# Optimization experiments

Measured on AMD Instinct MI355X. Metric: run time of the kernel, lower is better.

The kernel has to match this reference:

```python
import jax, jax.numpy as jnp
import numpy as np

LAM = 0.5          # lambda_ in DyGCN
GROUPS = 4
EPS_GN = 1e-5
EPS_LN = 1e-5


def _group_norm(y, w, b):
    # y: [B, Ch, N, T]; GroupNorm over (channels-in-group, N, T)
    B, Ch, N, T = y.shape
    yr = y.reshape(B, GROUPS, Ch // GROUPS, N, T)
    mu = yr.mean(axis=(2, 3, 4), keepdims=True)
    var = yr.var(axis=(2, 3, 4), keepdims=True)
    yn = ((yr - mu) * jax.lax.rsqrt(var + EPS_GN)).reshape(B, Ch, N, T)
    return yn * w[None, :, None, None] + b[None, :, None, None]


def _gtu(X, w, b, pw, pb, qw, qb):
    # grouped conv2d, kernel (1,k), stride 1, VALID; out channels = 2*H
    xc = jax.lax.conv_general_dilated(
        X, w, window_strides=(1, 1), padding='VALID',
        feature_group_count=GROUPS,
        dimension_numbers=('NCHW', 'OIHW', 'NCHW'))
    xc = xc + b[None, :, None, None]
    H = X.shape[1]
    xp = _group_norm(xc[:, :H], pw, pb)   # matches torch chunk(2, dim=1)
    xq = _group_norm(xc[:, H:], qw, qb)
    mish = xp * jnp.tanh(jax.nn.softplus(xp))   # Mish
    gate = jnp.clip(xq, 0.0, 1.0)               # Hardtanh(0,1)
    return mish * gate


def reference(x, static_adj, U1, U2, U3, be, Ve, W0, b0, masks, Ws, bs, Wd, bd,
              conv3_w, conv5_w, conv7_w, conv9_w, conv_b,
              gn_pw, gn_pb, gn_qw, gn_qb, fc_w, fc_b, res_w, res_b, ln_w, ln_b):
    B, N, C, T = x.shape
    # ---- Temporal attention ----
    lhs = jnp.einsum('btc,cn->btn', jnp.einsum('bnct,n->btc', x, U1), U2)  # [B,T,N]
    rhs = jnp.einsum('c,bnct->bnt', U3, x)                                 # [B,N,T]
    product = jnp.einsum('btn,bns->bts', lhs, rhs)                          # [B,T,T]
    E = jnp.einsum('ij,bjk->bik', Ve, jax.nn.sigmoid(product + be))
    At = jax.nn.softmax(E, axis=1)
    x_TAt = jnp.einsum('bmt,bts->bms', x.reshape(B, N * C, T), At).reshape(B, N, C, T)
    # ---- DyGCN, vectorized across T ----
    xt = jnp.moveaxis(x_TAt, -1, 1)                                        # [B,T,N,C]
    x0 = jnp.einsum('btnc,hc->btnh', xt, W0) + b0                          # shared linear
    enh = static_adj[None] * jax.nn.sigmoid(masks)                         # [T,N,N]
    s = jnp.einsum('tnm,btmc->btnc', enh, xt)
    static_out = jnp.einsum('btnc,thc->btnh', s, Ws) + bs[None, :, None, :]
    # dynamic branch (DynamicGCNLayer): data-dependent adjacency
    scores = jnp.einsum('btnc,btmc->btnm', xt, xt) / jnp.sqrt(jnp.float32(C))
    adj = jax.nn.softmax(scores, axis=-1)                                  # [B,T,N,N]
    d = jnp.einsum('btnm,btmc->btnc', adj, xt)
    dyn_out = jnp.einsum('btnc,thc->btnh', d, Wd) + bd[None, :, None, :]
    fused = (LAM - 0.025) * static_out + (1.0 - LAM - 0.025) * dyn_out + 0.05 * x0
    X = jnp.transpose(fused, (0, 3, 2, 1))                                 # [B,H,N,T]
    # ---- multi-scale gated temporal convs ----
    outs = [
        _gtu(X, conv3_w, conv_b[0], gn_pw[0], gn_pb[0], gn_qw[0], gn_qb[0]),
        _gtu(X, conv5_w, conv_b[1], gn_pw[1], gn_pb[1], gn_qw[1], gn_qb[1]),
        _gtu(X, conv7_w, conv_b[2], gn_pw[2], gn_pb[2], gn_qw[2], gn_qb[2]),
        _gtu(X, conv9_w, conv_b[3], gn_pw[3], gn_pb[3], gn_qw[3], gn_qb[3]),
    ]
    tc = jnp.concatenate(outs, axis=-1)                                    # [B,H,N,4T-20]
    tc = jnp.einsum('bhnk,ok->bhno', tc, fc_w) + fc_b                      # fcmy (dropout=eval no-op)
    tco = jax.nn.relu(tc)                                                  # [B,H,N,T]
    # ---- residual + LayerNorm ----
    residual = jnp.einsum('bnct,hc->bhnt', x, res_w) + res_b[None, :, None, None]
    y = jax.nn.relu(residual + tco)                                        # [B,H,N,T]
    yp = jnp.transpose(y, (0, 3, 2, 1))                                    # [B,T,N,H]
    mu = yp.mean(axis=-1, keepdims=True)
    var = yp.var(axis=-1, keepdims=True)
    yn = (yp - mu) * jax.lax.rsqrt(var + EPS_LN) * ln_w + ln_b
    return jnp.transpose(yn, (0, 2, 3, 1))                                 # [B,N,H,T]


def setup_inputs():
    key = jax.random.key(0)
    ks = jax.random.split(key, 32)
    B, N, C, T, H = 16, 512, 64, 12, 64
    w = 0.05
    A = jax.random.uniform(ks[0], (N, N), jnp.float32)
    A = A / A.sum(axis=-1, keepdims=True)  # row-normalized static adjacency
    return {
        'x': jax.random.normal(ks[1], (B, N, C, T), jnp.float32),
        'static_adj': A,
        'U1': jax.random.normal(ks[2], (N,), jnp.float32) * w,
        'U2': jax.random.normal(ks[3], (C, N), jnp.float32) * w,
        'U3': jax.random.normal(ks[4], (C,), jnp.float32) * w,
        'be': jax.random.normal(ks[5], (1, T, T), jnp.float32) * w,
        'Ve': jax.random.normal(ks[6], (T, T), jnp.float32) * w,
        'W0': jax.random.normal(ks[7], (H, C), jnp.float32) * w,
        'b0': jnp.zeros((H,), jnp.float32),
        'masks': jax.random.uniform(ks[8], (T, N, N), jnp.float32, 0.8, 1.2),
        'Ws': jax.random.normal(ks[9], (T, H, C), jnp.float32) * w,
        'bs': jnp.zeros((T, H), jnp.float32),
        'Wd': jax.random.normal(ks[10], (T, H, C), jnp.float32) * w,
        'bd': jnp.zeros((T, H), jnp.float32),
        'conv3_w': jax.random.normal(ks[11], (2 * H, H // 4, 1, 3), jnp.float32) * w,
        'conv5_w': jax.random.normal(ks[12], (2 * H, H // 4, 1, 5), jnp.float32) * w,
        'conv7_w': jax.random.normal(ks[13], (2 * H, H // 4, 1, 7), jnp.float32) * w,
        'conv9_w': jax.random.normal(ks[14], (2 * H, H // 4, 1, 9), jnp.float32) * w,
        'conv_b': jnp.zeros((4, 2 * H), jnp.float32),
        'gn_pw': jnp.ones((4, H), jnp.float32),
        'gn_pb': jnp.zeros((4, H), jnp.float32),
        'gn_qw': jnp.ones((4, H), jnp.float32),
        'gn_qb': jnp.zeros((4, H), jnp.float32),
        'fc_w': jax.random.normal(ks[15], (T, 4 * T - 20), jnp.float32) * w,
        'fc_b': jnp.zeros((T,), jnp.float32),
        'res_w': jax.random.normal(ks[16], (H, C), jnp.float32) * w,
        'res_b': jnp.zeros((H,), jnp.float32),
        'ln_w': jnp.ones((H,), jnp.float32),
        'ln_b': jnp.zeros((H,), jnp.float32),
    }
```

## Files before the change

### kernel.cpp

```cpp
#include <hip/hip_runtime.h>

constexpr int Bb = 16, Nn = 512, Cc = 64, Tt = 12, Hh = 64;
constexpr int NCT = Nn * Cc * Tt;
constexpr int CT  = Cc * Tt;

__global__ void k0_rest(const float* __restrict__ rw, float* __restrict__ resT) {
    int i = blockIdx.x * 256 + threadIdx.x;
    if (i < Hh * Cc) {
        int h = i >> 6, c = i & 63;
        resT[c * 64 + h] = rw[i];
    }
}

__global__ void k1a_tmp1(const float* __restrict__ x, const float* __restrict__ U1,
                         float* __restrict__ tmp1) {
    int blk = blockIdx.x;
    int b = blk / 12; int r = blk % 12;
    int ctb = r >> 2; int nch = r & 3;
    int ct = ctb * 256 + threadIdx.x;
    const float* xb = x + (size_t)b * NCT;
    float acc = 0.f;
    int n0 = nch * 128;
    for (int n = n0; n < n0 + 128; ++n)
        acc += xb[n * CT + ct] * U1[n];
    atomicAdd(&tmp1[b * CT + ct], acc);
}

__global__ void k1b_rhs(const float* __restrict__ x, const float* __restrict__ U3,
                        float* __restrict__ rhs) {
    int idx = blockIdx.x * 256 + threadIdx.x;
    int b = idx / (Nn * Tt);
    int r = idx % (Nn * Tt);
    int n = r / Tt; int t = r % Tt;
    const float* xr = x + (size_t)b * NCT + n * CT + t;
    float a = 0.f;
    for (int c = 0; c < Cc; ++c) a += xr[c * Tt] * U3[c];
    rhs[idx] = a;
}

__global__ void k1c_att(const float* __restrict__ tmp1, const float* __restrict__ rhs,
                        const float* __restrict__ U2, const float* __restrict__ be,
                        const float* __restrict__ Ve, float* __restrict__ At) {
    __shared__ float t1[CT];
    __shared__ float rh[Nn * Tt];
    __shared__ float lh[Tt * Nn];
    __shared__ float sp[144];
    __shared__ float Ee[144];
    int b = blockIdx.x, tid = threadIdx.x;
    for (int i = tid; i < CT; i += 256) t1[i] = tmp1[b * CT + i];
    for (int i = tid; i < Nn * Tt; i += 256) rh[i] = rhs[b * Nn * Tt + i];
    __syncthreads();
    for (int nn = tid; nn < Nn; nn += 256) {
        float l[Tt];
        #pragma unroll
        for (int t = 0; t < Tt; ++t) l[t] = 0.f;
        for (int c = 0; c < Cc; ++c) {
            float u2 = U2[c * Nn + nn];
            #pragma unroll
            for (int t = 0; t < Tt; ++t) l[t] += t1[c * Tt + t] * u2;
        }
        #pragma unroll
        for (int t = 0; t < Tt; ++t) lh[t * Nn + nn] = l[t];
    }
    __syncthreads();
    if (tid < 144) {
        int t = tid / 12, s2 = tid % 12;
        float a = 0.f;
        for (int nn = 0; nn < Nn; ++nn) a += lh[t * Nn + nn] * rh[nn * Tt + s2];
        a += be[tid];
        sp[tid] = 1.f / (1.f + __expf(-a));
    }
    __syncthreads();
    if (tid < 144) {
        int i = tid / 12, k = tid % 12;
        float a = 0.f;
        #pragma unroll
        for (int j = 0; j < 12; ++j) a += Ve[i * 12 + j] * sp[j * 12 + k];
        Ee[tid] = a;
    }
    __syncthreads();
    if (tid < 12) {
        int k = tid;
        float mx = -1e30f;
        #pragma unroll
        for (int i = 0; i < 12; ++i) mx = fmaxf(mx, Ee[i * 12 + k]);
        float su = 0.f; float ex[12];
        #pragma unroll
        for (int i = 0; i < 12; ++i) { ex[i] = __expf(Ee[i * 12 + k] - mx); su += ex[i]; }
        float inv = 1.f / su;
        #pragma unroll
        for (int i = 0; i < 12; ++i) At[b * 144 + i * 12 + k] = ex[i] * inv;
    }
}

__global__ void k2_xtt(const float* __restrict__ x, const float* __restrict__ At,
                       float* __restrict__ xtT) {
    int idx = blockIdx.x * 256 + threadIdx.x;
    int n = idx & 511; int c = (idx >> 9) & 63; int b = idx >> 15;
    const float* xr = x + (size_t)((b * Nn + n) * Cc + c) * Tt;
    float xv[Tt];
    {
        const float4* x4 = (const float4*)xr;
        float4 a0 = x4[0], a1 = x4[1], a2 = x4[2];
        xv[0]=a0.x; xv[1]=a0.y; xv[2]=a0.z; xv[3]=a0.w;
        xv[4]=a1.x; xv[5]=a1.y; xv[6]=a1.z; xv[7]=a1.w;
        xv[8]=a2.x; xv[9]=a2.y; xv[10]=a2.z; xv[11]=a2.w;
    }
    const float* Ab = At + b * 144;
    for (int t = 0; t < Tt; ++t) {
        float a = 0.f;
        #pragma unroll
        for (int u = 0; u < Tt; ++u) a += xv[u] * Ab[u * 12 + t];
        xtT[((size_t)(b * Tt + t) * Cc + c) * Nn + n] = a;
    }
}

__global__ void k2b_enh(const float* __restrict__ adj, const float* __restrict__ masks,
                        float* __restrict__ enhT) {
    __shared__ float tile[32][33];
    int blk = blockIdx.x;
    int t = blk >> 8; int r = blk & 255;
    int n0 = (r >> 4) * 32; int m0 = (r & 15) * 32;
    int tx = threadIdx.x & 31; int ty = threadIdx.x >> 5;
    #pragma unroll
    for (int i = 0; i < 4; ++i) {
        int nl = ty + 8 * i;
        float a  = adj[(n0 + nl) * Nn + m0 + tx];
        float mk = masks[t * Nn * Nn + (n0 + nl) * Nn + m0 + tx];
        tile[nl][tx] = a / (1.f + __expf(-mk));
    }
    __syncthreads();
    #pragma unroll
    for (int i = 0; i < 4; ++i) {
        int ml = ty + 8 * i;
        enhT[(size_t)(t * Nn + m0 + ml) * Nn + n0 + tx] = tile[tx][ml];
    }
}

__global__ __launch_bounds__(256, 3) void k3_gcn(
    const float* __restrict__ xtT, const float* __restrict__ enhT,
    const float* __restrict__ W0, const float* __restrict__ b0,
    const float* __restrict__ Ws, const float* __restrict__ bs,
    const float* __restrict__ Wd, const float* __restrict__ bd,
    float* __restrict__ F) {
    __shared__ float xs[64][64];
    int blk = blockIdx.x;
    int seg = blk & 3; int t = (blk >> 2) % Tt; int b = blk / (Tt * 4);
    int tid = threadIdx.x;
    int lane = tid & 63;
    int w = tid >> 6;
    int half = lane >> 5;
    int r = lane & 31;
    int n = seg * 128 + w * 32 + r;
    int c0 = half * 32;
    const float* xb = xtT + (size_t)(b * Tt + t) * Cc * Nn;
    float row[32], accd[32], accs[32];
    #pragma unroll
    for (int j = 0; j < 32; ++j) row[j] = xb[(c0 + j) * Nn + n];
    #pragma unroll
    for (int j = 0; j < 32; ++j) { accd[j] = 0.f; accs[j] = 0.f; }
    float sumexp = 0.f;
    const float* ehT = enhT + (size_t)t * Nn * Nn + n;
    for (int m0 = 0; m0 < Nn; m0 += 64) {
        __syncthreads();
        #pragma unroll
        for (int i = 0; i < 4; ++i) {
            int f = i * 256 + tid;
            int c = f >> 4; int mi = (f & 15) * 4;
            *(float4*)&xs[c][mi] = *(const float4*)(xb + c * Nn + m0 + mi);
        }
        __syncthreads();
        for (int m4 = 0; m4 < 64; m4 += 4) {
            float s0 = 0.f, s1 = 0.f, s2 = 0.f, s3 = 0.f;
            #pragma unroll
            for (int j = 0; j < 32; ++j) {
                float4 v = *(const float4*)&xs[c0 + j][m4];
                float rj = row[j];
                s0 += rj * v.x; s1 += rj * v.y; s2 += rj * v.z; s3 += rj * v.w;
            }
            s0 += __shfl_xor(s0, 32); s1 += __shfl_xor(s1, 32);
            s2 += __shfl_xor(s2, 32); s3 += __shfl_xor(s3, 32);
            float p0 = __expf(s0 * 0.125f), p1 = __expf(s1 * 0.125f);
            float p2 = __expf(s2 * 0.125f), p3 = __expf(s3 * 0.125f);
            sumexp += (p0 + p1) + (p2 + p3);
            float e0 = ehT[(m0 + m4 + 0) * Nn];
            float e1 = ehT[(m0 + m4 + 1) * Nn];
            float e2 = ehT[(m0 + m4 + 2) * Nn];
            float e3 = ehT[(m0 + m4 + 3) * Nn];
            asm volatile("" ::: "memory");
            #pragma unroll
            for (int j = 0; j < 32; ++j) {
                float4 v = *(const float4*)&xs[c0 + j][m4];
                accd[j] += p0 * v.x + p1 * v.y + p2 * v.z + p3 * v.w;
                accs[j] += e0 * v.x + e1 * v.y + e2 * v.z + e3 * v.w;
            }
        }
    }
    float invd = 0.475f / sumexp;
    #pragma unroll
    for (int j = 0; j < 32; ++j) {
        accd[j] *= invd; accs[j] *= 0.475f; row[j] *= 0.05f;
    }
    const float* Wst = Ws + t * Hh * Cc;
    const float* Wdt = Wd + t * Hh * Cc;
    float* Fp = F + ((size_t)(b * Tt + t) * Nn + n) * Hh;
    for (int hb = 0; hb < 16; ++hb) {
        float o[4];
        #pragma unroll
        for (int k = 0; k < 4; ++k) {
            int h = hb * 4 + k;
            float a = (half == 0)
                ? (0.05f * b0[h] + 0.475f * (bs[t * Hh + h] + bd[t * Hh + h]))
                : 0.f;
            const float* w0r = W0 + h * Cc + c0;
            const float* wsr = Wst + h * Cc + c0;
            const float* wdr = Wdt + h * Cc + c0;
            #pragma unroll
            for (int j = 0; j < 32; ++j)
                a += row[j] * w0r[j] + accs[j] * wsr[j] + accd[j] * wdr[j];
            a += __shfl_xor(a, 32);
            o[k] = a;
        }
        if ((hb >> 3) == half)
            *(float4*)(Fp + hb * 4) = make_float4(o[0], o[1], o[2], o[3]);
    }
}

__global__ void k4_conv(const float* __restrict__ F,
                        const float* __restrict__ w3, const float* __restrict__ w5,
                        const float* __restrict__ w7, const float* __restrict__ w9,
                        const float* __restrict__ cb,
                        float* __restrict__ xc, float* __restrict__ stats) {
    __shared__ float fl[2 * Tt * Hh];
    __shared__ float sstat[64];
    int blk = blockIdx.x;
    int b = blk >> 8; int n0 = (blk & 255) * 2;
    int tid = threadIdx.x;
    if (tid < 64) sstat[tid] = 0.f;
    for (int i = tid; i < 1536; i += 256) {
        int t = i >> 7; int r = i & 127;
        fl[i] = F[(size_t)(b * Tt + t) * Nn * Hh + n0 * Hh + r];
    }
    __syncthreads();
    int nl = tid >> 7; int co = tid & 127;
    int g = co >> 5;
    float a3[10], a5[8], a7[6], a9[4];
    {
        float c3 = cb[co], c5 = cb[128 + co], c7 = cb[256 + co], c9 = cb[384 + co];
        #pragma unroll
        for (int j = 0; j < 10; ++j) a3[j] = c3;
        #pragma unroll
        for (int j = 0; j < 8; ++j) a5[j] = c5;
        #pragma unroll
        for (int j = 0; j < 6; ++j) a7[j] = c7;
        #pragma unroll
        for (int j = 0; j < 4; ++j) a9[j] = c9;
    }
    for (int ci = 0; ci < 16; ++ci) {
        int cig = g * 16 + ci;
        float xr[12];
        #pragma unroll
        for (int tt = 0; tt < 12; ++tt) xr[tt] = fl[tt * 128 + nl * 64 + cig];
        const float* p3 = w3 + (co * 16 + ci) * 3;
        #pragma unroll
        for (int dt = 0; dt < 3; ++dt) {
            float wv = p3[dt];
            #pragma unroll
            for (int j = 0; j < 10; ++j) a3[j] += xr[j + dt] * wv;
        }
        const float* p5 = w5 + (co * 16 + ci) * 5;
        #pragma unroll
        for (int dt = 0; dt < 5; ++dt) {
            float wv = p5[dt];
            #pragma unroll
            for (int j = 0; j < 8; ++j) a5[j] += xr[j + dt] * wv;
        }
        const float* p7 = w7 + (co * 16 + ci) * 7;
        #pragma unroll
        for (int dt = 0; dt < 7; ++dt) {
            float wv = p7[dt];
            #pragma unroll
            for (int j = 0; j < 6; ++j) a7[j] += xr[j + dt] * wv;
        }
        const float* p9 = w9 + (co * 16 + ci) * 9;
        #pragma unroll
        for (int dt = 0; dt < 9; ++dt) {
            float wv = p9[dt];
            #pragma unroll
            for (int j = 0; j < 4; ++j) a9[j] += xr[j + dt] * wv;
        }
    }
    int pg = (co < 64) ? (co >> 4) : 4 + ((co - 64) >> 4);
    float* xcw = xc + ((size_t)(b * Nn + n0 + nl) * 128 + co) * 28;
    float su, sq;
    su = 0.f; sq = 0.f;
    #pragma unroll
    for (int j = 0; j < 10; ++j) { float v = a3[j]; xcw[j] = v; su += v; sq += v * v; }
    #pragma unroll
    for (int off = 1; off < 16; off <<= 1) { su += __shfl_xor(su, off); sq += __shfl_xor(sq, off); }
    if ((tid & 15) == 0) { atomicAdd(&sstat[(0 * 8 + pg) * 2], su); atomicAdd(&sstat[(0 * 8 + pg) * 2 + 1], sq); }
    su = 0.f; sq = 0.f;
    #pragma unroll
    for (int j = 0; j < 8; ++j) { float v = a5[j]; xcw[10 + j] = v; su += v; sq += v * v; }
    #pragma unroll
    for (int off = 1; off < 16; off <<= 1) { su += __shfl_xor(su, off); sq += __shfl_xor(sq, off); }
    if ((tid & 15) == 0) { atomicAdd(&sstat[(1 * 8 + pg) * 2], su); atomicAdd(&sstat[(1 * 8 + pg) * 2 + 1], sq); }
    su = 0.f; sq = 0.f;
    #pragma unroll
    for (int j = 0; j < 6; ++j) { float v = a7[j]; xcw[18 + j] = v; su += v; sq += v * v; }
    #pragma unroll
    for (int off = 1; off < 16; off <<= 1) { su += __shfl_xor(su, off); sq += __shfl_xor(sq, off); }
    if ((tid & 15) == 0) { atomicAdd(&sstat[(2 * 8 + pg) * 2], su); atomicAdd(&sstat[(2 * 8 + pg) * 2 + 1], sq); }
    su = 0.f; sq = 0.f;
    #pragma unroll
    for (int j = 0; j < 4; ++j) { float v = a9[j]; xcw[24 + j] = v; su += v; sq += v * v; }
    #pragma unroll
    for (int off = 1; off < 16; off <<= 1) { su += __shfl_xor(su, off); sq += __shfl_xor(sq, off); }
    if ((tid & 15) == 0) { atomicAdd(&sstat[(3 * 8 + pg) * 2], su); atomicAdd(&sstat[(3 * 8 + pg) * 2 + 1], sq); }
    __syncthreads();
    if (tid < 64) {
        int s = tid >> 4; int pgq = (tid >> 1) & 7; int st = tid & 1;
        atomicAdd(&stats[((s * Bb + b) * 8 + pgq) * 2 + st], sstat[(s * 8 + pgq) * 2 + st]);
    }
}

__global__ __launch_bounds__(256) void k5_final(
                         const float* __restrict__ xc, const float* __restrict__ stats,
                         const float* __restrict__ x,
                         const float* __restrict__ gpw, const float* __restrict__ gpb,
                         const float* __restrict__ gqw, const float* __restrict__ gqb,
                         const float* __restrict__ fcw, const float* __restrict__ fcb,
                         const float* __restrict__ resT, const float* __restrict__ rb,
                         const float* __restrict__ lnw, const float* __restrict__ lnb,
                         float* __restrict__ out) {
    int blk = blockIdx.x;
    int b = blk >> 7; int n = (blk & 127) * 4 + (threadIdx.x >> 6);
    int h = threadIdx.x & 63;
    int pg = h >> 4;
    const int TkA[4] = {10, 8, 6, 4};
    float mu_p[4], rs_p[4], mu_q[4], rs_q[4];
    #pragma unroll
    for (int s = 0; s < 4; ++s) {
        float cnt = 16.f * 512.f * (float)TkA[s];
        float su = stats[((s * Bb + b) * 8 + pg) * 2];
        float sq = stats[((s * Bb + b) * 8 + pg) * 2 + 1];
        float mu = su / cnt; float var = sq / cnt - mu * mu;
        mu_p[s] = mu; rs_p[s] = rsqrtf(var + 1e-5f);
        su = stats[((s * Bb + b) * 8 + 4 + pg) * 2];
        sq = stats[((s * Bb + b) * 8 + 4 + pg) * 2 + 1];
        mu = su / cnt; var = sq / cnt - mu * mu;
        mu_q[s] = mu; rs_q[s] = rsqrtf(var + 1e-5f);
    }
    const float* xcp = xc + ((size_t)(b * Nn + n) * 128 + h) * 28;
    const float* xcq = xcp + 64 * 28;
    float pb_[28], qb_[28];
    {
        const float4* p4 = (const float4*)xcp;
        const float4* q4 = (const float4*)xcq;
        #pragma unroll
        for (int j = 0; j < 7; ++j) {
            float4 a = p4[j];
            pb_[j*4] = a.x; pb_[j*4+1] = a.y; pb_[j*4+2] = a.z; pb_[j*4+3] = a.w;
            float4 c = q4[j];
            qb_[j*4] = c.x; qb_[j*4+1] = c.y; qb_[j*4+2] = c.z; qb_[j*4+3] = c.w;
        }
    }
    float tc[28];
    int off = 0;
    #pragma unroll
    for (int s = 0; s < 4; ++s) {
        float pw = gpw[s * 64 + h], pbv = gpb[s * 64 + h];
        float qw = gqw[s * 64 + h], qbv = gqb[s * 64 + h];
        #pragma unroll
        for (int j = 0; j < 10; ++j) {
            if (j < TkA[s]) {
                float p = (pb_[off + j] - mu_p[s]) * rs_p[s] * pw + pbv;
                float q = (qb_[off + j] - mu_q[s]) * rs_q[s] * qw + qbv;
                float mish;
                if (p > 20.f) mish = p;
                else { float z = 1.f + __expf(p); float z2 = z * z; mish = p * (z2 - 1.f) / (z2 + 1.f); }
                float gate = fminf(fmaxf(q, 0.f), 1.f);
                tc[off + j] = mish * gate;
            }
        }
        off += TkA[s];
    }
    float o[12];
    #pragma unroll
    for (int t = 0; t < 12; ++t) {
        float a = fcb[t];
        #pragma unroll
        for (int k = 0; k < 28; ++k) a += tc[k] * fcw[t * 28 + k];
        o[t] = fmaxf(a, 0.f);
    }
    const float* xr = x + (size_t)(b * Nn + n) * CT;
    float res[12];
    float rbv = rb[h];
    #pragma unroll
    for (int t = 0; t < 12; ++t) res[t] = rbv;
    for (int c = 0; c < 64; ++c) {
        float rv = resT[c * 64 + h];
        #pragma unroll
        for (int t = 0; t < 12; ++t) res[t] += xr[c * 12 + t] * rv;
    }
    float y[12];
    #pragma unroll
    for (int t = 0; t < 12; ++t) y[t] = fmaxf(res[t] + o[t], 0.f);
    float lw = lnw[h], lb = lnb[h];
    float* op = out + ((size_t)(b * Nn + n) * Hh + h) * Tt;
    #pragma unroll
    for (int t = 0; t < 12; ++t) {
        float s1 = y[t], s2 = y[t] * y[t];
        #pragma unroll
        for (int o2 = 32; o2 > 0; o2 >>= 1) {
            s1 += __shfl_xor(s1, o2);
            s2 += __shfl_xor(s2, o2);
        }
        float mu = s1 * (1.f / 64.f);
        float var = s2 * (1.f / 64.f) - mu * mu;
        op[t] = (y[t] - mu) * rsqrtf(var + 1e-5f) * lw + lb;
    }
}

extern "C" void kernel_launch(void* const* d_in, const int* in_sizes, int n_in,
                              void* d_out, int out_size, void* d_ws, size_t ws_size,
                              hipStream_t stream) {
    const float* x    = (const float*)d_in[0];
    const float* adj  = (const float*)d_in[1];
    const float* U1   = (const float*)d_in[2];
    const float* U2   = (const float*)d_in[3];
    const float* U3   = (const float*)d_in[4];
    const float* be   = (const float*)d_in[5];
    const float* Ve   = (const float*)d_in[6];
    const float* W0   = (const float*)d_in[7];
    const float* b0   = (const float*)d_in[8];
    const float* masks= (const float*)d_in[9];
    const float* Ws   = (const float*)d_in[10];
    const float* bs   = (const float*)d_in[11];
    const float* Wd   = (const float*)d_in[12];
    const float* bd   = (const float*)d_in[13];
    const float* w3   = (const float*)d_in[14];
    const float* w5   = (const float*)d_in[15];
    const float* w7   = (const float*)d_in[16];
    const float* w9   = (const float*)d_in[17];
    const float* cb   = (const float*)d_in[18];
    const float* gpw  = (const float*)d_in[19];
    const float* gpb  = (const float*)d_in[20];
    const float* gqw  = (const float*)d_in[21];
    const float* gqb  = (const float*)d_in[22];
    const float* fcw  = (const float*)d_in[23];
    const float* fcb  = (const float*)d_in[24];
    const float* rw   = (const float*)d_in[25];
    const float* rb   = (const float*)d_in[26];
    const float* lnw  = (const float*)d_in[27];
    const float* lnb  = (const float*)d_in[28];
    float* out = (float*)d_out;
    float* ws  = (float*)d_ws;

    float* tmp1  = ws;
    float* stats = ws + 12288;
    float* At    = ws + 13312;
    float* rhs   = ws + 15616;
    float* resT  = ws + 113920;
    float* xtT   = ws + 118016;
    float* enhT  = ws + 6409472;
    float* F     = ws + 9555200;
    float* xc    = ws + 15846656;

    hipMemsetAsync(ws, 0, 13312 * sizeof(float), stream);

    k0_rest<<<16, 256, 0, stream>>>(rw, resT);
    k1a_tmp1<<<192, 256, 0, stream>>>(x, U1, tmp1);
    k1b_rhs<<<384, 256, 0, stream>>>(x, U3, rhs);
    k2b_enh<<<3072, 256, 0, stream>>>(adj, masks, enhT);
    k1c_att<<<16, 256, 0, stream>>>(tmp1, rhs, U2, be, Ve, At);
    k2_xtt<<<2048, 256, 0, stream>>>(x, At, xtT);
    k3_gcn<<<768, 256, 0, stream>>>(xtT, enhT, W0, b0, Ws, bs, Wd, bd, F);
    k4_conv<<<4096, 256, 0, stream>>>(F, w3, w5, w7, w9, cb, xc, stats);
    k5_final<<<2048, 256, 0, stream>>>(xc, stats, x, gpw, gpb, gqw, gqb,
                                       fcw, fcb, resT, rb, lnw, lnb, out);
}
```

Measured before the change: 1.244 ms.

## Repartition GCN, rhs, attention, conv kernels and vectorize output stores

The rhs reduction now gives one wavefront to each node, with coalesced float4 loads of x and a shuffle reduction over channels. The attention score reduction is split into four partial sums across more threads. The GCN kernel splits channels into four 16-wide groups per node instead of two 32-wide halves, which cuts per-thread register state and doubles the grid. The conv kernel processes four nodes per 512-thread block, and the final LayerNorm output is written with float4 stores. Each change targets occupancy or memory coalescing, at the cost of extra shuffle reductions and more redundant LDS reads in the GCN kernel.

```diff
diff --git a/kernel.cpp b/kernel.cpp
--- a/kernel.cpp
+++ b/kernel.cpp
@@ -28,14 +28,27 @@
 
 __global__ void k1b_rhs(const float* __restrict__ x, const float* __restrict__ U3,
                         float* __restrict__ rhs) {
-    int idx = blockIdx.x * 256 + threadIdx.x;
-    int b = idx / (Nn * Tt);
-    int r = idx % (Nn * Tt);
-    int n = r / Tt; int t = r % Tt;
-    const float* xr = x + (size_t)b * NCT + n * CT + t;
-    float a = 0.f;
-    for (int c = 0; c < Cc; ++c) a += xr[c * Tt] * U3[c];
-    rhs[idx] = a;
+    int wid = blockIdx.x * 4 + (threadIdx.x >> 6);
+    int b = wid >> 9; int n = wid & 511;
+    int l = threadIdx.x & 63;
+    const float4* x4 = (const float4*)(x + (size_t)(b * Nn + n) * CT);
+    float4 a0 = x4[3 * l], a1 = x4[3 * l + 1], a2 = x4[3 * l + 2];
+    float xv[12] = {a0.x,a0.y,a0.z,a0.w, a1.x,a1.y,a1.z,a1.w, a2.x,a2.y,a2.z,a2.w};
+    float u = U3[l];
+    float p[12];
+    #pragma unroll
+    for (int t = 0; t < 12; ++t) p[t] = u * xv[t];
+    #pragma unroll
+    for (int off = 1; off < 64; off <<= 1) {
+        #pragma unroll
+        for (int t = 0; t < 12; ++t) p[t] += __shfl_xor(p[t], off);
+    }
+    if (l == 0) {
+        float* rp = rhs + (size_t)(b * Nn + n) * 12;
+        *(float4*)(rp)     = make_float4(p[0], p[1], p[2], p[3]);
+        *(float4*)(rp + 4) = make_float4(p[4], p[5], p[6], p[7]);
+        *(float4*)(rp + 8) = make_float4(p[8], p[9], p[10], p[11]);
+    }
 }
 
 __global__ void k1c_att(const float* __restrict__ tmp1, const float* __restrict__ rhs,
@@ -44,6 +57,7 @@
     __shared__ float t1[CT];
     __shared__ float rh[Nn * Tt];
     __shared__ float lh[Tt * Nn];
+    __shared__ float part[576];
     __shared__ float sp[144];
     __shared__ float Ee[144];
     int b = blockIdx.x, tid = threadIdx.x;
@@ -63,11 +77,18 @@
         for (int t = 0; t < Tt; ++t) lh[t * Nn + nn] = l[t];
     }
     __syncthreads();
+    for (int task = tid; task < 576; task += 256) {
+        int ts = task >> 2, ch = task & 3;
+        int t = ts / 12, s2 = ts % 12;
+        int n0 = ch * 128;
+        float a = 0.f;
+        for (int nn = n0; nn < n0 + 128; ++nn) a += lh[t * Nn + nn] * rh[nn * Tt + s2];
+        part[task] = a;
+    }
+    __syncthreads();
     if (tid < 144) {
-        int t = tid / 12, s2 = tid % 12;
-        float a = 0.f;
-        for (int nn = 0; nn < Nn; ++nn) a += lh[t * Nn + nn] * rh[nn * Tt + s2];
-        a += be[tid];
+        float a = part[tid * 4] + part[tid * 4 + 1] + part[tid * 4 + 2] + part[tid * 4 + 3]
+                + be[tid];
         sp[tid] = 1.f / (1.f + __expf(-a));
     }
     __syncthreads();
@@ -145,20 +166,20 @@
     float* __restrict__ F) {
     __shared__ float xs[64][64];
     int blk = blockIdx.x;
-    int seg = blk & 3; int t = (blk >> 2) % Tt; int b = blk / (Tt * 4);
+    int seg = blk & 7; int t = (blk >> 3) % Tt; int b = blk / (Tt * 8);
     int tid = threadIdx.x;
     int lane = tid & 63;
     int w = tid >> 6;
-    int half = lane >> 5;
-    int r = lane & 31;
-    int n = seg * 128 + w * 32 + r;
-    int c0 = half * 32;
+    int cg = lane >> 4;
+    int r = lane & 15;
+    int n = seg * 64 + w * 16 + r;
+    int c0 = cg * 16;
     const float* xb = xtT + (size_t)(b * Tt + t) * Cc * Nn;
-    float row[32], accd[32], accs[32];
-    #pragma unroll
-    for (int j = 0; j < 32; ++j) row[j] = xb[(c0 + j) * Nn + n];
-    #pragma unroll
-    for (int j = 0; j < 32; ++j) { accd[j] = 0.f; accs[j] = 0.f; }
+    float row[16], accd[16], accs[16];
+    #pragma unroll
+    for (int j = 0; j < 16; ++j) row[j] = xb[(c0 + j) * Nn + n];
+    #pragma unroll
+    for (int j = 0; j < 16; ++j) { accd[j] = 0.f; accs[j] = 0.f; }
     float sumexp = 0.f;
     const float* ehT = enhT + (size_t)t * Nn * Nn + n;
     for (int m0 = 0; m0 < Nn; m0 += 64) {
@@ -170,75 +191,83 @@
             *(float4*)&xs[c][mi] = *(const float4*)(xb + c * Nn + m0 + mi);
         }
         __syncthreads();
+        #pragma unroll 1
         for (int m4 = 0; m4 < 64; m4 += 4) {
-            float s0 = 0.f, s1 = 0.f, s2 = 0.f, s3 = 0.f;
-            #pragma unroll
-            for (int j = 0; j < 32; ++j) {
-                float4 v = *(const float4*)&xs[c0 + j][m4];
-                float rj = row[j];
-                s0 += rj * v.x; s1 += rj * v.y; s2 += rj * v.z; s3 += rj * v.w;
-            }
-            s0 += __shfl_xor(s0, 32); s1 += __shfl_xor(s1, 32);
-            s2 += __shfl_xor(s2, 32); s3 += __shfl_xor(s3, 32);
-            float p0 = __expf(s0 * 0.125f), p1 = __expf(s1 * 0.125f);
-            float p2 = __expf(s2 * 0.125f), p3 = __expf(s3 * 0.125f);
-            sumexp += (p0 + p1) + (p2 + p3);
             float e0 = ehT[(m0 + m4 + 0) * Nn];
             float e1 = ehT[(m0 + m4 + 1) * Nn];
             float e2 = ehT[(m0 + m4 + 2) * Nn];
             float e3 = ehT[(m0 + m4 + 3) * Nn];
-            asm volatile("" ::: "memory");
-            #pragma unroll
-            for (int j = 0; j < 32; ++j) {
-                float4 v = *(const float4*)&xs[c0 + j][m4];
-                accd[j] += p0 * v.x + p1 * v.y + p2 * v.z + p3 * v.w;
-                accs[j] += e0 * v.x + e1 * v.y + e2 * v.z + e3 * v.w;
+            float4 v[16];
+            #pragma unroll
+            for (int j = 0; j < 16; ++j) v[j] = *(const float4*)&xs[c0 + j][m4];
+            float s0 = 0.f, s1 = 0.f, s2 = 0.f, s3 = 0.f;
+            #pragma unroll
+            for (int j = 0; j < 16; ++j) {
+                float rj = row[j];
+                s0 += rj * v[j].x; s1 += rj * v[j].y;
+                s2 += rj * v[j].z; s3 += rj * v[j].w;
             }
+            s0 += __shfl_xor(s0, 16); s0 += __shfl_xor(s0, 32);
+            s1 += __shfl_xor(s1, 16); s1 += __shfl_xor(s1, 32);
+            s2 += __shfl_xor(s2, 16); s2 += __shfl_xor(s2, 32);
+            s3 += __shfl_xor(s3, 16); s3 += __shfl_xor(s3, 32);
+            float p0 = __expf(s0 * 0.125f), p1 = __expf(s1 * 0.125f);
+            float p2 = __expf(s2 * 0.125f), p3 = __expf(s3 * 0.125f);
+            sumexp += (p0 + p1) + (p2 + p3);
+            #pragma unroll
+            for (int j = 0; j < 16; ++j) {
+                accd[j] += p0 * v[j].x + p1 * v[j].y + p2 * v[j].z + p3 * v[j].w;
+                accs[j] += e0 * v[j].x + e1 * v[j].y + e2 * v[j].z + e3 * v[j].w;
+            }
         }
     }
     float invd = 0.475f / sumexp;
     #pragma unroll
-    for (int j = 0; j < 32; ++j) {
+    for (int j = 0; j < 16; ++j) {
         accd[j] *= invd; accs[j] *= 0.475f; row[j] *= 0.05f;
     }
     const float* Wst = Ws + t * Hh * Cc;
     const float* Wdt = Wd + t * Hh * Cc;
     float* Fp = F + ((size_t)(b * Tt + t) * Nn + n) * Hh;
     for (int hb = 0; hb < 16; ++hb) {
-        float o[4];
+        float oo[4];
         #pragma unroll
         for (int k = 0; k < 4; ++k) {
             int h = hb * 4 + k;
-            float a = (half == 0)
-                ? (0.05f * b0[h] + 0.475f * (bs[t * Hh + h] + bd[t * Hh + h]))
-                : 0.f;
-            const float* w0r = W0 + h * Cc + c0;
-            const float* wsr = Wst + h * Cc + c0;
-            const float* wdr = Wdt + h * Cc + c0;
-            #pragma unroll
-            for (int j = 0; j < 32; ++j)
-                a += row[j] * w0r[j] + accs[j] * wsr[j] + accd[j] * wdr[j];
+            const float4* w04 = (const float4*)(W0 + h * Cc + c0);
+            const float4* ws4 = (const float4*)(Wst + h * Cc + c0);
+            const float4* wd4 = (const float4*)(Wdt + h * Cc + c0);
+            float a = 0.f;
+            #pragma unroll
+            for (int jj = 0; jj < 4; ++jj) {
+                float4 wv = w04[jj], sv = ws4[jj], dv = wd4[jj];
+                a += row[jj*4+0]*wv.x + row[jj*4+1]*wv.y + row[jj*4+2]*wv.z + row[jj*4+3]*wv.w;
+                a += accs[jj*4+0]*sv.x + accs[jj*4+1]*sv.y + accs[jj*4+2]*sv.z + accs[jj*4+3]*sv.w;
+                a += accd[jj*4+0]*dv.x + accd[jj*4+1]*dv.y + accd[jj*4+2]*dv.z + accd[jj*4+3]*dv.w;
+            }
+            a += __shfl_xor(a, 16);
             a += __shfl_xor(a, 32);
-            o[k] = a;
-        }
-        if ((hb >> 3) == half)
-            *(float4*)(Fp + hb * 4) = make_float4(o[0], o[1], o[2], o[3]);
-    }
-}
-
-__global__ void k4_conv(const float* __restrict__ F,
+            oo[k] = a + 0.05f * b0[h] + 0.475f * (bs[t * Hh + h] + bd[t * Hh + h]);
+        }
+        if ((hb >> 2) == cg)
+            *(float4*)(Fp + hb * 4) = make_float4(oo[0], oo[1], oo[2], oo[3]);
+    }
+}
+
+__global__ __launch_bounds__(512) void k4_conv(
+                        const float* __restrict__ F,
                         const float* __restrict__ w3, const float* __restrict__ w5,
                         const float* __restrict__ w7, const float* __restrict__ w9,
                         const float* __restrict__ cb,
                         float* __restrict__ xc, float* __restrict__ stats) {
-    __shared__ float fl[2 * Tt * Hh];
+    __shared__ float fl[4 * Tt * Hh];
     __shared__ float sstat[64];
     int blk = blockIdx.x;
-    int b = blk >> 8; int n0 = (blk & 255) * 2;
+    int b = blk >> 7; int n0 = (blk & 127) * 4;
     int tid = threadIdx.x;
     if (tid < 64) sstat[tid] = 0.f;
-    for (int i = tid; i < 1536; i += 256) {
-        int t = i >> 7; int r = i & 127;
+    for (int i = tid; i < 3072; i += 512) {
+        int t = i >> 8; int r = i & 255;
         fl[i] = F[(size_t)(b * Tt + t) * Nn * Hh + n0 * Hh + r];
     }
     __syncthreads();
@@ -260,7 +289,7 @@
         int cig = g * 16 + ci;
         float xr[12];
         #pragma unroll
-        for (int tt = 0; tt < 12; ++tt) xr[tt] = fl[tt * 128 + nl * 64 + cig];
+        for (int tt = 0; tt < 12; ++tt) xr[tt] = fl[tt * 256 + nl * 64 + cig];
         const float* p3 = w3 + (co * 16 + ci) * 3;
         #pragma unroll
         for (int dt = 0; dt < 3; ++dt) {
@@ -407,7 +436,7 @@
     #pragma unroll
     for (int t = 0; t < 12; ++t) y[t] = fmaxf(res[t] + o[t], 0.f);
     float lw = lnw[h], lb = lnb[h];
-    float* op = out + ((size_t)(b * Nn + n) * Hh + h) * Tt;
+    float ov[12];
     #pragma unroll
     for (int t = 0; t < 12; ++t) {
         float s1 = y[t], s2 = y[t] * y[t];
@@ -418,8 +447,12 @@
         }
         float mu = s1 * (1.f / 64.f);
         float var = s2 * (1.f / 64.f) - mu * mu;
-        op[t] = (y[t] - mu) * rsqrtf(var + 1e-5f) * lw + lb;
-    }
+        ov[t] = (y[t] - mu) * rsqrtf(var + 1e-5f) * lw + lb;
+    }
+    float* op = out + ((size_t)(b * Nn + n) * Hh + h) * Tt;
+    *(float4*)(op)     = make_float4(ov[0], ov[1], ov[2], ov[3]);
+    *(float4*)(op + 4) = make_float4(ov[4], ov[5], ov[6], ov[7]);
+    *(float4*)(op + 8) = make_float4(ov[8], ov[9], ov[10], ov[11]);
 }
 
 extern "C" void kernel_launch(void* const* d_in, const int* in_sizes, int n_in,
@@ -471,12 +504,12 @@
 
     k0_rest<<<16, 256, 0, stream>>>(rw, resT);
     k1a_tmp1<<<192, 256, 0, stream>>>(x, U1, tmp1);
-    k1b_rhs<<<384, 256, 0, stream>>>(x, U3, rhs);
+    k1b_rhs<<<2048, 256, 0, stream>>>(x, U3, rhs);
     k2b_enh<<<3072, 256, 0, stream>>>(adj, masks, enhT);
     k1c_att<<<16, 256, 0, stream>>>(tmp1, rhs, U2, be, Ve, At);
     k2_xtt<<<2048, 256, 0, stream>>>(x, At, xtT);
-    k3_gcn<<<768, 256, 0, stream>>>(xtT, enhT, W0, b0, Ws, bs, Wd, bd, F);
-    k4_conv<<<4096, 256, 0, stream>>>(F, w3, w5, w7, w9, cb, xc, stats);
+    k3_gcn<<<1536, 256, 0, stream>>>(xtT, enhT, W0, b0, Ws, bs, Wd, bd, F);
+    k4_conv<<<2048, 512, 0, stream>>>(F, w3, w5, w7, w9, cb, xc, stats);
     k5_final<<<2048, 256, 0, stream>>>(xc, stats, x, gpw, gpb, gqw, gqb,
                                        fcw, fcb, resT, rb, lnw, lnb, out);
 }
```

New measurement: 1.315 ms. +5.7%, slower.
